# Kernel optimization log

Hardware: AMD Instinct MI355X
Metric: run time of the kernel (lower is better)

The kernel has to match this reference:

```python
import jax, jax.numpy as jnp
import numpy as np

N = 100000   # nodes
C = 64       # num_channels
E = 1250000  # edges


def _linear_params(key, c):
    k1, k2 = jax.random.split(key)
    s = 1.0 / np.sqrt(c)
    W = jax.random.uniform(k1, (c, c), minval=-s, maxval=s, dtype=jnp.float32)
    b = jax.random.uniform(k2, (c,), minval=-s, maxval=s, dtype=jnp.float32)
    return W, b


def setup_inputs() -> dict:
    key = jax.random.key(0)
    ks = jax.random.split(key, 10)
    W_ig, b_ig = _linear_params(ks[0], C)    # input_gate
    W_og, b_og = _linear_params(ks[1], C)    # output_gate
    W_in, b_in = _linear_params(ks[2], C)    # self.input
    W_gw, b_gw = _linear_params(ks[3], C)    # self.gw
    W_out, b_out = _linear_params(ks[4], C)  # self.out
    W_arma, _ = _linear_params(ks[5], C)     # ARMA init_weight [C, C]
    V_arma, b_arma = _linear_params(ks[6], C)  # ARMA root_weight + bias
    x = jax.random.normal(ks[7], (N, C), dtype=jnp.float32)
    edge_index = jax.random.randint(ks[8], (2, E), 0, N, dtype=jnp.int32)
    return dict(x=x, edge_index=edge_index,
                W_ig=W_ig, b_ig=b_ig, W_og=W_og, b_og=b_og,
                W_in=W_in, b_in=b_in, W_arma=W_arma, V_arma=V_arma,
                b_arma=b_arma, W_gw=W_gw, b_gw=b_gw, W_out=W_out, b_out=b_out)


def _arma_conv(h, edge_index, W_arma, V_arma, b_arma):
    # ARMAConv(K=1, T=1): out = ReLU(L_hat @ (h @ W) + h @ V + b)
    # L_hat = D^{-1/2} A D^{-1/2}, gcn_norm without self-loops.
    row, col = edge_index[0], edge_index[1]  # source, target
    deg = jax.ops.segment_sum(jnp.ones((E,), h.dtype), col, num_segments=N)
    dis = jnp.where(deg > 0, jax.lax.rsqrt(jnp.maximum(deg, 1.0)), 0.0)
    norm = dis[row] * dis[col]                       # [E]
    m = h @ W_arma                                   # [N, C]
    agg = jax.ops.segment_sum(norm[:, None] * m[row], col, num_segments=N)
    return jax.nn.relu(agg + h @ V_arma + b_arma)


def reference(x, edge_index, W_ig, b_ig, W_og, b_og, W_in, b_in,
              W_arma, V_arma, b_arma, W_gw, b_gw, W_out, b_out):
    input_gate = jax.nn.sigmoid(x @ W_ig + b_ig)
    output_gate = jax.nn.sigmoid(x @ W_og + b_og)
    h = input_gate * x
    h = jax.nn.gelu(h @ W_in + b_in, approximate=False)
    h = _arma_conv(h, edge_index, W_arma, V_arma, b_arma)
    h = jax.nn.gelu(h @ W_gw + b_gw, approximate=False)
    h = h @ W_out + b_out
    return output_gate * h
```

## Files before the change

kernel.cpp:

```cpp
#include <hip/hip_runtime.h>
#include <hip/hip_fp16.h>
#include <math.h>

#define NN 100000
#define CC 64
#define EE 1250000
#define NTILE 6250
#define CAP 48

#define NSUB 256
#define SUBSZ 391
#define NPB 512
#define EPCB ((EE + NPB - 1) / NPB)
#define LCAP 28
#define RBCAP2 5400

using f32x4 = __attribute__((ext_vector_type(4))) float;
using s16x8 = __attribute__((ext_vector_type(8))) short;

__device__ __forceinline__ float sigmoidf_(float v) {
    return __builtin_amdgcn_rcpf(1.0f + __expf(-v));
}
__device__ __forceinline__ float gelu_(float v) {
    float s = fabsf(v) * 0.70710678118654752440f;
    float t = __builtin_amdgcn_rcpf(fmaf(0.3275911f, s, 1.0f));
    float poly = fmaf(fmaf(fmaf(fmaf(1.061405429f, t, -1.453152027f),
                               t, 1.421413741f), t, -0.284496736f), t, 0.254829592f) * t;
    float er = 1.0f - poly * __expf(-s * s);
    er = copysignf(er, v);
    return 0.5f * v * (1.0f + er);
}

__device__ __forceinline__ unsigned short bfr(float f) {
    unsigned u = __float_as_uint(f);
    return (unsigned short)((u + 0x7FFFu + ((u >> 16) & 1u)) >> 16);
}
__device__ __forceinline__ float bf2f(unsigned short h) {
    return __uint_as_float(((unsigned)h) << 16);
}
__device__ __forceinline__ void split8(const float* f, s16x8& hi, s16x8& lo) {
    #pragma unroll
    for (int j = 0; j < 8; j++) {
        unsigned short h = bfr(f[j]);
        hi[j] = (short)h;
        lo[j] = (short)bfr(f[j] - bf2f(h));
    }
}

__device__ __forceinline__ int swz4(int r, int u) { return r * 64 + (((u ^ r) & 15) << 2); }
__device__ __forceinline__ int swz1(int r, int c) {
    return r * 64 + (((((c >> 2) ^ r) & 15) << 2) | (c & 3));
}

__global__ void zero_kernel(unsigned* __restrict__ p, int n) {
    int i = blockIdx.x * blockDim.x + threadIdx.x;
    if (i < n) p[i] = 0u;
}

__global__ __launch_bounds__(256) void part_kernel(
    const int* __restrict__ ei,
    unsigned long long* __restrict__ rbuf,
    unsigned* __restrict__ rcur)
{
    __shared__ unsigned long long lbuf[NSUB * LCAP];
    __shared__ unsigned lcnt[NSUB];
    __shared__ unsigned pref[NSUB];
    __shared__ unsigned lbase[NSUB];

    const int t = threadIdx.x;
    lcnt[t] = 0;
    __syncthreads();

    const int e0 = blockIdx.x * EPCB;
    int e1 = e0 + EPCB; if (e1 > EE) e1 = EE;
    for (int e = e0 + t; e < e1; e += 256) {
        int c = ei[EE + e];
        int r = ei[e];
        int s = c / SUBSZ;
        unsigned long long pk = ((unsigned long long)(unsigned)c << 32) | (unsigned)r;
        unsigned pos = atomicAdd(&lcnt[s], 1u);
        if (pos < (unsigned)LCAP) {
            lbuf[s * LCAP + pos] = pk;
        } else {
            unsigned gp = atomicAdd(&rcur[s], 1u);
            if (gp < (unsigned)RBCAP2) rbuf[(size_t)s * RBCAP2 + gp] = pk;
        }
    }
    __syncthreads();

    unsigned v = lcnt[t]; if (v > (unsigned)LCAP) v = LCAP;
    __syncthreads();
    lcnt[t] = v;
    pref[t] = v;
    __syncthreads();
    #pragma unroll
    for (int o = 1; o < 256; o <<= 1) {
        unsigned u = (t >= o) ? pref[t - o] : 0u;
        __syncthreads();
        pref[t] += u;
        __syncthreads();
    }
    unsigned incl  = pref[t];
    unsigned total = pref[NSUB - 1];
    lbase[t] = atomicAdd(&rcur[t], v);
    __syncthreads();
    pref[t] = incl - v;
    __syncthreads();

    for (unsigned i = t; i < total; i += 256) {
        int lo = 0, hi = NSUB - 1;
        while (lo < hi) {
            int mid = (lo + hi + 1) >> 1;
            if (pref[mid] <= i) lo = mid; else hi = mid - 1;
        }
        unsigned pos = i - pref[lo];
        unsigned dst = lbase[lo] + pos;
        if (dst < (unsigned)RBCAP2)
            rbuf[(size_t)lo * RBCAP2 + dst] = lbuf[lo * LCAP + pos];
    }
}

__global__ __launch_bounds__(256) void fill3_kernel(
    const unsigned long long* __restrict__ rbuf,
    const unsigned* __restrict__ rcur,
    unsigned* __restrict__ cnt,
    int* __restrict__ srcs)
{
    __shared__ int bucket[SUBSZ * CAP];
    __shared__ unsigned bcnt[SUBSZ];
    const int s = blockIdx.x;
    const int base = s * SUBSZ;

    for (int i = threadIdx.x; i < SUBSZ; i += 256) bcnt[i] = 0;
    __syncthreads();

    unsigned total = rcur[s];
    if (total > (unsigned)RBCAP2) total = RBCAP2;
    const unsigned long long* rb = rbuf + (size_t)s * RBCAP2;
    for (unsigned i = threadIdx.x; i < total; i += 256) {
        unsigned long long pk = rb[i];
        int c = (int)(pk >> 32);
        int r = (int)(pk & 0xffffffffu);
        unsigned slot = atomicAdd(&bcnt[c - base], 1u);
        if (slot < (unsigned)CAP) bucket[(c - base) * CAP + slot] = r;
    }
    __syncthreads();

    for (int i = threadIdx.x; i < SUBSZ; i += 256) {
        int node = base + i;
        if (node < NN) cnt[node] = bcnt[i];
    }
    int4* dst = (int4*)(srcs + (size_t)base * CAP);
    const int4* src = (const int4*)bucket;
    const int nv = SUBSZ * CAP / 4;
    for (int i = threadIdx.x; i < nv; i += 256) dst[i] = src[i];
}

__global__ __launch_bounds__(256) void gather_kernel(
    const unsigned* __restrict__ cnt,
    const int* __restrict__ srcs,
    const __half2* __restrict__ mp2, float* __restrict__ z)
{
    const int wid  = (blockIdx.x * 256 + threadIdx.x) >> 6;
    const int lane = threadIdx.x & 63;
    const int node = wid * 2 + (lane >> 5);
    const int ch2  = lane & 31;
    if (node >= NN) return;

    unsigned d = cnt[node];
    float dn = (d > 0u) ? rsqrtf((float)d) : 0.0f;
    unsigned n = (d > (unsigned)CAP) ? (unsigned)CAP : d;
    const int* sp = srcs + (size_t)node * CAP;

    float2 a0 = {0.f, 0.f}, a1 = {0.f, 0.f}, a2 = {0.f, 0.f}, a3 = {0.f, 0.f};
    unsigned e = 0;
    for (; e + 4 <= n; e += 4) {
        int r0 = sp[e], r1 = sp[e + 1], r2 = sp[e + 2], r3 = sp[e + 3];
        float2 v0 = __half22float2(mp2[(size_t)r0 * 32 + ch2]);
        float2 v1 = __half22float2(mp2[(size_t)r1 * 32 + ch2]);
        float2 v2 = __half22float2(mp2[(size_t)r2 * 32 + ch2]);
        float2 v3 = __half22float2(mp2[(size_t)r3 * 32 + ch2]);
        a0.x += v0.x; a0.y += v0.y;
        a1.x += v1.x; a1.y += v1.y;
        a2.x += v2.x; a2.y += v2.y;
        a3.x += v3.x; a3.y += v3.y;
    }
    if (e + 2 <= n) {
        int r0 = sp[e], r1 = sp[e + 1];
        float2 v0 = __half22float2(mp2[(size_t)r0 * 32 + ch2]);
        float2 v1 = __half22float2(mp2[(size_t)r1 * 32 + ch2]);
        a0.x += v0.x; a0.y += v0.y;
        a1.x += v1.x; a1.y += v1.y;
        e += 2;
    }
    if (e < n) {
        float2 v0 = __half22float2(mp2[(size_t)sp[e] * 32 + ch2]);
        a2.x += v0.x; a2.y += v0.y;
    }

    float sx = (a0.x + a1.x) + (a2.x + a3.x);
    float sy = (a0.y + a1.y) + (a2.y + a3.y);
    float2* zp = (float2*)(z + (size_t)node * 64 + 2 * ch2);
    float2 zv = *zp;
    zv.x += dn * sx;
    zv.y += dn * sy;
    *zp = zv;
}


#define MFMA(a, b, c) __builtin_amdgcn_mfma_f32_16x16x32_bf16(a, b, c, 0, 0, 0)

__global__ __launch_bounds__(1024) void k12_mfma(
    const float* __restrict__ x,
    const float* __restrict__ Wig, const float* __restrict__ big,
    const float* __restrict__ Wog, const float* __restrict__ bog,
    const float* __restrict__ Win, const float* __restrict__ bin,
    const float* __restrict__ Wa,  const float* __restrict__ Va,
    const float* __restrict__ ba,  const unsigned* __restrict__ cnt,
    __half* __restrict__ og_out, __half* __restrict__ mp_out, float* __restrict__ z_out)
{
    __shared__ s16x8 wh[5 * 512];
    __shared__ s16x8 wl[5 * 512];
    __shared__ float xs[16][1024];

    const float* Ws[5] = {Wig, Wog, Win, Wa, Va};
    for (int s = threadIdx.x; s < 5 * 512; s += 1024) {
        int mat = s >> 9, sub = s & 511;
        int fi = sub >> 6, ln = sub & 63;
        int ct = fi >> 1, kc = fi & 1;
        const float* W = Ws[mat];
        int ks = kc * 32 + (ln >> 4) * 8;
        int ch = ct * 16 + (ln & 15);
        float f[8];
        #pragma unroll
        for (int j = 0; j < 8; j++) f[j] = W[(ks + j) * 64 + ch];
        s16x8 hi, lo; split8(f, hi, lo);
        wh[s] = hi; wl[s] = lo;
    }
    __syncthreads();

    const int wv = threadIdx.x >> 6, l = threadIdx.x & 63;
    const int tile = blockIdx.x * 16 + wv;
    if (tile >= NTILE) return;
    const int R = tile * 16;
    const int la = l & 15, g = l >> 4;
    float* xw = xs[wv];

    const float* xp = x + (size_t)(R + la) * 64;
    float xf[16];
    {
        f32x4 a = *(const f32x4*)(xp + g * 8);
        f32x4 b = *(const f32x4*)(xp + g * 8 + 4);
        f32x4 c = *(const f32x4*)(xp + 32 + g * 8);
        f32x4 d = *(const f32x4*)(xp + 32 + g * 8 + 4);
        int u0 = g * 2, u1 = 8 + g * 2;
        *(f32x4*)&xw[swz4(la, u0)]     = a;
        *(f32x4*)&xw[swz4(la, u0 + 1)] = b;
        *(f32x4*)&xw[swz4(la, u1)]     = c;
        *(f32x4*)&xw[swz4(la, u1 + 1)] = d;
        #pragma unroll
        for (int j = 0; j < 4; j++) {
            xf[j] = a[j]; xf[4 + j] = b[j]; xf[8 + j] = c[j]; xf[12 + j] = d[j];
        }
    }
    s16x8 ah0, al0, ah1, al1;
    split8(xf, ah0, al0); split8(xf + 8, ah1, al1);

    f32x4 aig[4], aog[4];
    #pragma unroll
    for (int ct = 0; ct < 4; ct++) {
        float b0 = big[ct * 16 + la], b1 = bog[ct * 16 + la];
        aig[ct] = (f32x4){b0, b0, b0, b0};
        aog[ct] = (f32x4){b1, b1, b1, b1};
    }
    #pragma unroll
    for (int ct = 0; ct < 4; ct++) {
        #pragma unroll
        for (int kc = 0; kc < 2; kc++) {
            s16x8 ah = kc ? ah1 : ah0, al = kc ? al1 : al0;
            int fi = (0 * 8 + ct * 2 + kc) * 64 + l;
            s16x8 bh = wh[fi], bl = wl[fi];
            aig[ct] = MFMA(ah, bh, aig[ct]);
            aig[ct] = MFMA(al, bh, aig[ct]);
            aig[ct] = MFMA(ah, bl, aig[ct]);
            int fo = (1 * 8 + ct * 2 + kc) * 64 + l;
            bh = wh[fo]; bl = wl[fo];
            aog[ct] = MFMA(ah, bh, aog[ct]);
            aog[ct] = MFMA(al, bh, aog[ct]);
            aog[ct] = MFMA(ah, bl, aog[ct]);
        }
    }
    __builtin_amdgcn_sched_barrier(0);

    #pragma unroll
    for (int ct = 0; ct < 4; ct++) {
        int ch = ct * 16 + la;
        #pragma unroll
        for (int r = 0; r < 4; r++) {
            int rr = 4 * g + r;
            float igv = sigmoidf_(aig[ct][r]);
            float ogv = sigmoidf_(aog[ct][r]);
            og_out[(size_t)(R + rr) * 64 + ch] = __float2half(ogv);
            int si = swz1(rr, ch);
            xw[si] = igv * xw[si];
        }
    }
    __builtin_amdgcn_sched_barrier(0);

    float hf[16];
    {
        int u0 = g * 2, u1 = 8 + g * 2;
        f32x4 a = *(const f32x4*)&xw[swz4(la, u0)];
        f32x4 b = *(const f32x4*)&xw[swz4(la, u0 + 1)];
        f32x4 c = *(const f32x4*)&xw[swz4(la, u1)];
        f32x4 d = *(const f32x4*)&xw[swz4(la, u1 + 1)];
        #pragma unroll
        for (int j = 0; j < 4; j++) {
            hf[j] = a[j]; hf[4 + j] = b[j]; hf[8 + j] = c[j]; hf[12 + j] = d[j];
        }
    }
    split8(hf, ah0, al0); split8(hf + 8, ah1, al1);

    f32x4 ain[4];
    #pragma unroll
    for (int ct = 0; ct < 4; ct++) {
        float b0 = bin[ct * 16 + la];
        ain[ct] = (f32x4){b0, b0, b0, b0};
    }
    #pragma unroll
    for (int ct = 0; ct < 4; ct++) {
        #pragma unroll
        for (int kc = 0; kc < 2; kc++) {
            s16x8 ah = kc ? ah1 : ah0, al = kc ? al1 : al0;
            int fi = (2 * 8 + ct * 2 + kc) * 64 + l;
            s16x8 bh = wh[fi], bl = wl[fi];
            ain[ct] = MFMA(ah, bh, ain[ct]);
            ain[ct] = MFMA(al, bh, ain[ct]);
            ain[ct] = MFMA(ah, bl, ain[ct]);
        }
    }
    __builtin_amdgcn_sched_barrier(0);

    #pragma unroll
    for (int ct = 0; ct < 4; ct++) {
        int ch = ct * 16 + la;
        #pragma unroll
        for (int r = 0; r < 4; r++)
            xw[swz1(4 * g + r, ch)] = gelu_(ain[ct][r]);
    }
    __builtin_amdgcn_sched_barrier(0);

    {
        int u0 = g * 2, u1 = 8 + g * 2;
        f32x4 a = *(const f32x4*)&xw[swz4(la, u0)];
        f32x4 b = *(const f32x4*)&xw[swz4(la, u0 + 1)];
        f32x4 c = *(const f32x4*)&xw[swz4(la, u1)];
        f32x4 d = *(const f32x4*)&xw[swz4(la, u1 + 1)];
        #pragma unroll
        for (int j = 0; j < 4; j++) {
            hf[j] = a[j]; hf[4 + j] = b[j]; hf[8 + j] = c[j]; hf[12 + j] = d[j];
        }
    }
    split8(hf, ah0, al0); split8(hf + 8, ah1, al1);

    f32x4 am[4], az[4];
    #pragma unroll
    for (int ct = 0; ct < 4; ct++) {
        float b0 = ba[ct * 16 + la];
        am[ct] = (f32x4){0.0f, 0.0f, 0.0f, 0.0f};
        az[ct] = (f32x4){b0, b0, b0, b0};
    }
    #pragma unroll
    for (int ct = 0; ct < 4; ct++) {
        #pragma unroll
        for (int kc = 0; kc < 2; kc++) {
            s16x8 ah = kc ? ah1 : ah0, al = kc ? al1 : al0;
            int fa = (3 * 8 + ct * 2 + kc) * 64 + l;
            s16x8 bh = wh[fa], bl = wl[fa];
            am[ct] = MFMA(ah, bh, am[ct]);
            am[ct] = MFMA(al, bh, am[ct]);
            am[ct] = MFMA(ah, bl, am[ct]);
            int fv = (4 * 8 + ct * 2 + kc) * 64 + l;
            bh = wh[fv]; bl = wl[fv];
            az[ct] = MFMA(ah, bh, az[ct]);
            az[ct] = MFMA(al, bh, az[ct]);
            az[ct] = MFMA(ah, bl, az[ct]);
        }
    }

    f32x4 dv;
    {
        uint4 c4 = *(const uint4*)(cnt + R + 4 * g);
        unsigned cu[4] = {c4.x, c4.y, c4.z, c4.w};
        #pragma unroll
        for (int r = 0; r < 4; r++)
            dv[r] = (cu[r] > 0u) ? rsqrtf((float)cu[r]) : 0.0f;
    }
    #pragma unroll
    for (int ct = 0; ct < 4; ct++) {
        int ch = ct * 16 + la;
        #pragma unroll
        for (int r = 0; r < 4; r++) {
            size_t idx = (size_t)(R + 4 * g + r) * 64 + ch;
            mp_out[idx] = __float2half(dv[r] * am[ct][r]);
            z_out[idx]  = az[ct][r];
        }
    }
}

__global__ __launch_bounds__(512) void k3_mfma(
    const float* __restrict__ z, const __half* __restrict__ og,
    const float* __restrict__ Wgw, const float* __restrict__ bgw,
    const float* __restrict__ Wout, const float* __restrict__ bout,
    float* __restrict__ out)
{
    __shared__ s16x8 wh[2 * 512];
    __shared__ s16x8 wl[2 * 512];
    __shared__ float xs[8][1024];

    const float* Ws[2] = {Wgw, Wout};
    for (int s = threadIdx.x; s < 2 * 512; s += 512) {
        int mat = s >> 9, sub = s & 511;
        int fi = sub >> 6, ln = sub & 63;
        int ct = fi >> 1, kc = fi & 1;
        const float* W = Ws[mat];
        int ks = kc * 32 + (ln >> 4) * 8;
        int ch = ct * 16 + (ln & 15);
        float f[8];
        #pragma unroll
        for (int j = 0; j < 8; j++) f[j] = W[(ks + j) * 64 + ch];
        s16x8 hi, lo; split8(f, hi, lo);
        wh[s] = hi; wl[s] = lo;
    }
    __syncthreads();

    const int wv = threadIdx.x >> 6, l = threadIdx.x & 63;
    const int tile = blockIdx.x * 8 + wv;
    if (tile >= NTILE) return;
    const int R = tile * 16;
    const int la = l & 15, g = l >> 4;
    float* xw = xs[wv];

    const float* zp = z + (size_t)(R + la) * 64;
    float hf[16];
    {
        f32x4 a = *(const f32x4*)(zp + g * 8);
        f32x4 b = *(const f32x4*)(zp + g * 8 + 4);
        f32x4 c = *(const f32x4*)(zp + 32 + g * 8);
        f32x4 d = *(const f32x4*)(zp + 32 + g * 8 + 4);
        #pragma unroll
        for (int j = 0; j < 4; j++) {
            hf[j]      = fmaxf(a[j], 0.0f);
            hf[4 + j]  = fmaxf(b[j], 0.0f);
            hf[8 + j]  = fmaxf(c[j], 0.0f);
            hf[12 + j] = fmaxf(d[j], 0.0f);
        }
    }
    s16x8 ah0, al0, ah1, al1;
    split8(hf, ah0, al0); split8(hf + 8, ah1, al1);

    f32x4 ag[4];
    #pragma unroll
    for (int ct = 0; ct < 4; ct++) {
        float b0 = bgw[ct * 16 + la];
        ag[ct] = (f32x4){b0, b0, b0, b0};
    }
    #pragma unroll
    for (int ct = 0; ct < 4; ct++) {
        #pragma unroll
        for (int kc = 0; kc < 2; kc++) {
            s16x8 ah = kc ? ah1 : ah0, al = kc ? al1 : al0;
            int fi = (0 * 8 + ct * 2 + kc) * 64 + l;
            s16x8 bh = wh[fi], bl = wl[fi];
            ag[ct] = MFMA(ah, bh, ag[ct]);
            ag[ct] = MFMA(al, bh, ag[ct]);
            ag[ct] = MFMA(ah, bl, ag[ct]);
        }
    }
    __builtin_amdgcn_sched_barrier(0);

    #pragma unroll
    for (int ct = 0; ct < 4; ct++) {
        int ch = ct * 16 + la;
        #pragma unroll
        for (int r = 0; r < 4; r++)
            xw[swz1(4 * g + r, ch)] = gelu_(ag[ct][r]);
    }
    __builtin_amdgcn_sched_barrier(0);

    {
        int u0 = g * 2, u1 = 8 + g * 2;
        f32x4 a = *(const f32x4*)&xw[swz4(la, u0)];
        f32x4 b = *(const f32x4*)&xw[swz4(la, u0 + 1)];
        f32x4 c = *(const f32x4*)&xw[swz4(la, u1)];
        f32x4 d = *(const f32x4*)&xw[swz4(la, u1 + 1)];
        #pragma unroll
        for (int j = 0; j < 4; j++) {
            hf[j] = a[j]; hf[4 + j] = b[j]; hf[8 + j] = c[j]; hf[12 + j] = d[j];
        }
    }
    split8(hf, ah0, al0); split8(hf + 8, ah1, al1);

    f32x4 ao[4];
    #pragma unroll
    for (int ct = 0; ct < 4; ct++) {
        float b0 = bout[ct * 16 + la];
        ao[ct] = (f32x4){b0, b0, b0, b0};
    }
    #pragma unroll
    for (int ct = 0; ct < 4; ct++) {
        #pragma unroll
        for (int kc = 0; kc < 2; kc++) {
            s16x8 ah = kc ? ah1 : ah0, al = kc ? al1 : al0;
            int fi = (1 * 8 + ct * 2 + kc) * 64 + l;
            s16x8 bh = wh[fi], bl = wl[fi];
            ao[ct] = MFMA(ah, bh, ao[ct]);
            ao[ct] = MFMA(al, bh, ao[ct]);
            ao[ct] = MFMA(ah, bl, ao[ct]);
        }
    }
    #pragma unroll
    for (int ct = 0; ct < 4; ct++) {
        int ch = ct * 16 + la;
        #pragma unroll
        for (int r = 0; r < 4; r++) {
            size_t idx = (size_t)(R + 4 * g + r) * 64 + ch;
            out[idx] = __half2float(og[idx]) * ao[ct][r];
        }
    }
}

extern "C" void kernel_launch(void* const* d_in, const int* in_sizes, int n_in,
                              void* d_out, int out_size, void* d_ws, size_t ws_size,
                              hipStream_t stream) {
    const float* x      = (const float*)d_in[0];
    const int*   ei     = (const int*)d_in[1];
    const float* W_ig   = (const float*)d_in[2];
    const float* b_ig   = (const float*)d_in[3];
    const float* W_og   = (const float*)d_in[4];
    const float* b_og   = (const float*)d_in[5];
    const float* W_in   = (const float*)d_in[6];
    const float* b_in   = (const float*)d_in[7];
    const float* W_arma = (const float*)d_in[8];
    const float* V_arma = (const float*)d_in[9];
    const float* b_arma = (const float*)d_in[10];
    const float* W_gw   = (const float*)d_in[11];
    const float* b_gw   = (const float*)d_in[12];
    const float* W_out  = (const float*)d_in[13];
    const float* b_out  = (const float*)d_in[14];

    float* out = (float*)d_out;

    char* ws = (char*)d_ws;
    size_t off = 0;
    float* z       = (float*)(ws + off); off += (size_t)NN * CC * 4;
    __half* og     = (__half*)(ws + off); off += (size_t)NN * CC * 2;
    __half* mp     = (__half*)(ws + off); off += (size_t)NN * CC * 2;
    unsigned* cnt  = (unsigned*)(ws + off); off += (size_t)(NN + 32) * 4;
    unsigned* rcur = (unsigned*)(ws + off); off += (size_t)NSUB * 4 + 64;
    int* srcs      = (int*)(ws + off); off += (size_t)NSUB * SUBSZ * CAP * 4;
    unsigned long long* rbuf = (unsigned long long*)(ws + off);

    zero_kernel<<<1, NSUB, 0, stream>>>(rcur, NSUB);
    part_kernel<<<NPB, 256, 0, stream>>>(ei, rbuf, rcur);
    fill3_kernel<<<NSUB, 256, 0, stream>>>(rbuf, rcur, cnt, srcs);

    k12_mfma<<<(NTILE + 15) / 16, 1024, 0, stream>>>(x, W_ig, b_ig, W_og, b_og,
                                                     W_in, b_in, W_arma, V_arma,
                                                     b_arma, cnt, og, mp, z);

    gather_kernel<<<(NN / 2 * 64 + 255) / 256, 256, 0, stream>>>(
        cnt, srcs, (const __half2*)mp, z);

    k3_mfma<<<(NTILE + 7) / 8, 512, 0, stream>>>(z, og, W_gw, b_gw, W_out, b_out, out);
}
```

Before: 131.5 us.

## Fuse neighbor gather into final MFMA kernel via shared-memory staging

Removes the separate gather kernel and performs the per-node neighbor aggregation inside the final MFMA kernel. Each wave gathers its 16-row tile two nodes at a time, adds the result to z, and writes it into swizzled LDS, from which the MFMA stage reads directly. This drops one launch and the write-then-reread round trip of z through global memory. The cost is serialized gather work per wave (8 iterations) in a 512-thread block with large LDS, which may lower occupancy and the latency hiding available to the random gathers.

```diff
diff --git a/kernel.cpp b/kernel.cpp
--- a/kernel.cpp
+++ b/kernel.cpp
@@ -156,57 +156,6 @@
     for (int i = threadIdx.x; i < nv; i += 256) dst[i] = src[i];
 }
 
-__global__ __launch_bounds__(256) void gather_kernel(
-    const unsigned* __restrict__ cnt,
-    const int* __restrict__ srcs,
-    const __half2* __restrict__ mp2, float* __restrict__ z)
-{
-    const int wid  = (blockIdx.x * 256 + threadIdx.x) >> 6;
-    const int lane = threadIdx.x & 63;
-    const int node = wid * 2 + (lane >> 5);
-    const int ch2  = lane & 31;
-    if (node >= NN) return;
-
-    unsigned d = cnt[node];
-    float dn = (d > 0u) ? rsqrtf((float)d) : 0.0f;
-    unsigned n = (d > (unsigned)CAP) ? (unsigned)CAP : d;
-    const int* sp = srcs + (size_t)node * CAP;
-
-    float2 a0 = {0.f, 0.f}, a1 = {0.f, 0.f}, a2 = {0.f, 0.f}, a3 = {0.f, 0.f};
-    unsigned e = 0;
-    for (; e + 4 <= n; e += 4) {
-        int r0 = sp[e], r1 = sp[e + 1], r2 = sp[e + 2], r3 = sp[e + 3];
-        float2 v0 = __half22float2(mp2[(size_t)r0 * 32 + ch2]);
-        float2 v1 = __half22float2(mp2[(size_t)r1 * 32 + ch2]);
-        float2 v2 = __half22float2(mp2[(size_t)r2 * 32 + ch2]);
-        float2 v3 = __half22float2(mp2[(size_t)r3 * 32 + ch2]);
-        a0.x += v0.x; a0.y += v0.y;
-        a1.x += v1.x; a1.y += v1.y;
-        a2.x += v2.x; a2.y += v2.y;
-        a3.x += v3.x; a3.y += v3.y;
-    }
-    if (e + 2 <= n) {
-        int r0 = sp[e], r1 = sp[e + 1];
-        float2 v0 = __half22float2(mp2[(size_t)r0 * 32 + ch2]);
-        float2 v1 = __half22float2(mp2[(size_t)r1 * 32 + ch2]);
-        a0.x += v0.x; a0.y += v0.y;
-        a1.x += v1.x; a1.y += v1.y;
-        e += 2;
-    }
-    if (e < n) {
-        float2 v0 = __half22float2(mp2[(size_t)sp[e] * 32 + ch2]);
-        a2.x += v0.x; a2.y += v0.y;
-    }
-
-    float sx = (a0.x + a1.x) + (a2.x + a3.x);
-    float sy = (a0.y + a1.y) + (a2.y + a3.y);
-    float2* zp = (float2*)(z + (size_t)node * 64 + 2 * ch2);
-    float2 zv = *zp;
-    zv.x += dn * sx;
-    zv.y += dn * sy;
-    *zp = zv;
-}
-
 
 #define MFMA(a, b, c) __builtin_amdgcn_mfma_f32_16x16x32_bf16(a, b, c, 0, 0, 0)
 
@@ -408,7 +357,10 @@
     }
 }
 
-__global__ __launch_bounds__(512) void k3_mfma(
+__global__ __launch_bounds__(512) void k3g_mfma(
+    const unsigned* __restrict__ cnt,
+    const int* __restrict__ srcs,
+    const __half2* __restrict__ mp2,
     const float* __restrict__ z, const __half* __restrict__ og,
     const float* __restrict__ Wgw, const float* __restrict__ bgw,
     const float* __restrict__ Wout, const float* __restrict__ bout,
@@ -441,13 +393,58 @@
     const int la = l & 15, g = l >> 4;
     float* xw = xs[wv];
 
-    const float* zp = z + (size_t)(R + la) * 64;
+    const int half = l >> 5;
+    const int ch2  = l & 31;
+    #pragma unroll
+    for (int p = 0; p < 8; p++) {
+        int rr = 2 * p + half;
+        int node = R + rr;
+        unsigned d = cnt[node];
+        float dn = (d > 0u) ? rsqrtf((float)d) : 0.0f;
+        unsigned n = (d > (unsigned)CAP) ? (unsigned)CAP : d;
+        const int* sp = srcs + (size_t)node * CAP;
+
+        float2 a0 = {0.f, 0.f}, a1 = {0.f, 0.f}, a2 = {0.f, 0.f}, a3 = {0.f, 0.f};
+        unsigned e = 0;
+        for (; e + 4 <= n; e += 4) {
+            int r0 = sp[e], r1 = sp[e + 1], r2 = sp[e + 2], r3 = sp[e + 3];
+            float2 v0 = __half22float2(mp2[(size_t)r0 * 32 + ch2]);
+            float2 v1 = __half22float2(mp2[(size_t)r1 * 32 + ch2]);
+            float2 v2 = __half22float2(mp2[(size_t)r2 * 32 + ch2]);
+            float2 v3 = __half22float2(mp2[(size_t)r3 * 32 + ch2]);
+            a0.x += v0.x; a0.y += v0.y;
+            a1.x += v1.x; a1.y += v1.y;
+            a2.x += v2.x; a2.y += v2.y;
+            a3.x += v3.x; a3.y += v3.y;
+        }
+        if (e + 2 <= n) {
+            int r0 = sp[e], r1 = sp[e + 1];
+            float2 v0 = __half22float2(mp2[(size_t)r0 * 32 + ch2]);
+            float2 v1 = __half22float2(mp2[(size_t)r1 * 32 + ch2]);
+            a0.x += v0.x; a0.y += v0.y;
+            a1.x += v1.x; a1.y += v1.y;
+            e += 2;
+        }
+        if (e < n) {
+            float2 v0 = __half22float2(mp2[(size_t)sp[e] * 32 + ch2]);
+            a2.x += v0.x; a2.y += v0.y;
+        }
+        float sx = (a0.x + a1.x) + (a2.x + a3.x);
+        float sy = (a0.y + a1.y) + (a2.y + a3.y);
+
+        float2 zv = *(const float2*)(z + (size_t)node * 64 + 2 * ch2);
+        zv.x += dn * sx;
+        zv.y += dn * sy;
+        *(float2*)&xw[swz1(rr, 2 * ch2)] = zv;
+    }
+
     float hf[16];
     {
-        f32x4 a = *(const f32x4*)(zp + g * 8);
-        f32x4 b = *(const f32x4*)(zp + g * 8 + 4);
-        f32x4 c = *(const f32x4*)(zp + 32 + g * 8);
-        f32x4 d = *(const f32x4*)(zp + 32 + g * 8 + 4);
+        int u0 = g * 2, u1 = 8 + g * 2;
+        f32x4 a = *(const f32x4*)&xw[swz4(la, u0)];
+        f32x4 b = *(const f32x4*)&xw[swz4(la, u0 + 1)];
+        f32x4 c = *(const f32x4*)&xw[swz4(la, u1)];
+        f32x4 d = *(const f32x4*)&xw[swz4(la, u1 + 1)];
         #pragma unroll
         for (int j = 0; j < 4; j++) {
             hf[j]      = fmaxf(a[j], 0.0f);
@@ -569,8 +566,6 @@
                                                      W_in, b_in, W_arma, V_arma,
                                                      b_arma, cnt, og, mp, z);
 
-    gather_kernel<<<(NN / 2 * 64 + 255) / 256, 256, 0, stream>>>(
-        cnt, srcs, (const __half2*)mp, z);
-
-    k3_mfma<<<(NTILE + 7) / 8, 512, 0, stream>>>(z, og, W_gw, b_gw, W_out, b_out, out);
-}
+    k3g_mfma<<<(NTILE + 7) / 8, 512, 0, stream>>>(cnt, srcs, (const __half2*)mp,
+                                                  z, og, W_gw, b_gw, W_out, b_out, out);
+}
```

Result: slower. 150.3 us (+14.3%).
